# Optimization experiments

Measured on AMD Instinct MI355X. Metric: run time of the kernel, lower is better.

## Reference

```python
import jax, jax.numpy as jnp
import numpy as np

B, N_IN, D_IN, N_OUT, D_OUT, ROUTINGS = 512, 1152, 8, 10, 16, 3


def squash(s, axis=-1):
    # scale = |s|^2 / (1 + |s|^2) / (|s| + 1e-8)
    norm = jnp.linalg.norm(s, axis=axis, keepdims=True)
    return (norm ** 2 / (1.0 + norm ** 2) / (norm + 1e-8)) * s


def setup_inputs() -> dict:
    key = jax.random.key(0)
    k1, k2 = jax.random.split(key)
    x = jax.random.normal(k1, (B, N_IN, D_IN), dtype=jnp.float32)
    weight = 0.01 * jax.random.normal(k2, (N_OUT, N_IN, D_OUT, D_IN), dtype=jnp.float32)
    return {"x": x, "weight": weight}


def reference(x, weight):
    # x: [B, N_IN, D_IN]; weight: [N_OUT, N_IN, D_OUT, D_IN]
    # x_hat[b,o,n,:] = weight[o,n] @ x[b,n]  -> [B, N_OUT, N_IN, D_OUT]
    x_hat = jnp.einsum('onij,bnj->boni', weight, x)
    x_hat_det = jax.lax.stop_gradient(x_hat)

    # routing logits b: [B, N_OUT, N_IN]
    b = jnp.zeros(x_hat.shape[:3], dtype=x_hat.dtype)
    outputs = None
    for i in range(ROUTINGS):
        c = jax.nn.softmax(b, axis=1)  # softmax over output capsules
        if i == ROUTINGS - 1:
            outputs = squash(jnp.sum(c[..., None] * x_hat, axis=2))  # [B, N_OUT, D_OUT]
        else:
            outputs = squash(jnp.sum(c[..., None] * x_hat_det, axis=2))
            # agreement: b += <outputs, x_hat_det> over D_OUT
            b = b + jnp.einsum('bod,bond->bon', outputs, x_hat_det)
    return outputs  # [B, N_OUT, D_OUT]
```

## Files before the change

### kernel.cpp

```cpp
#include <hip/hip_runtime.h>
#include <hip/hip_bf16.h>
#include <hip/hip_fp16.h>

#define B_    512
#define NI    1152
#define NO    10
#define BT    16
#define NBT   32
#define NC    24
#define NCH   48
#define RNDS  6
#define RN    8

typedef __attribute__((ext_vector_type(8))) short bf16x8;
typedef __attribute__((ext_vector_type(4))) float f32x4;
typedef __attribute__((ext_vector_type(8))) unsigned short u16x8;

#define SPART_H    ((size_t)NC * NBT * NO * 256)
#define OUTSUM_F32 ((size_t)NBT * NO * 256)
#define XB_US      ((size_t)NBT * NC * RNDS * 1024)
#define WB_US      ((size_t)NC * RNDS * 12288)
#define WB2_US     ((size_t)NC * 12 * NO * 512)

__device__ inline unsigned short f2bf(float f) {
    __hip_bfloat16 h = __float2bfloat16(f);
    return *reinterpret_cast<unsigned short*>(&h);
}

__device__ __forceinline__ bf16x8 load_cvt8(const float* src) {
    f32x4 v0 = *reinterpret_cast<const f32x4*>(src);
    f32x4 v1 = *reinterpret_cast<const f32x4*>(src + 4);
    u16x8 u = { f2bf(v0[0]), f2bf(v0[1]), f2bf(v0[2]), f2bf(v0[3]),
                f2bf(v1[0]), f2bf(v1[1]), f2bf(v1[2]), f2bf(v1[3]) };
    return *reinterpret_cast<bf16x8*>(&u);
}

__device__ __forceinline__ void iter_epilogue(
    uint2 (*red)[NO * 64], const f32x4* sacc, float sc,
    int w, int l, int tid, unsigned short* base)
{
    #pragma unroll
    for (int o = 0; o < NO; ++o) {
        __half2 h01 = __floats2half2_rn(sacc[o][0] * sc, sacc[o][1] * sc);
        __half2 h23 = __floats2half2_rn(sacc[o][2] * sc, sacc[o][3] * sc);
        red[w][o * 64 + l] =
            make_uint2(*reinterpret_cast<unsigned int*>(&h01),
                       *reinterpret_cast<unsigned int*>(&h23));
    }
    __syncthreads();
    for (int g = tid; g < NO * 64; g += 256) {
        uint2 a0 = red[0][g], a1 = red[1][g], a2 = red[2][g], a3 = red[3][g];
        auto h2f2 = [](unsigned int u) {
            __half2 h = *reinterpret_cast<__half2*>(&u);
            return __half22float2(h);
        };
        float2 lo = h2f2(a0.x), l1 = h2f2(a1.x), l2 = h2f2(a2.x), l3 = h2f2(a3.x);
        float2 ho = h2f2(a0.y), h1 = h2f2(a1.y), h2 = h2f2(a2.y), h3 = h2f2(a3.y);
        float2 sl = { (lo.x + l1.x) + (l2.x + l3.x), (lo.y + l1.y) + (l2.y + l3.y) };
        float2 sh = { (ho.x + h1.x) + (h2.x + h3.x), (ho.y + h1.y) + (h2.y + h3.y) };
        __half2 p01 = __floats2half2_rn(sl.x, sl.y);
        __half2 p23 = __floats2half2_rn(sh.x, sh.y);
        *reinterpret_cast<uint2*>(base + (size_t)g * 4) =
            make_uint2(*reinterpret_cast<unsigned int*>(&p01),
                       *reinterpret_cast<unsigned int*>(&p23));
    }
}

__global__ __launch_bounds__(256) void cvt_xw(
    const float* __restrict__ x, const float* __restrict__ w,
    unsigned short* __restrict__ xb, unsigned short* __restrict__ wb,
    unsigned short* __restrict__ wb2)
{
    const int blk = blockIdx.x;
    if (blk < 2304) {
        const int t = blk * 256 + threadIdx.x;
        const int m   = t & 127;
        const int img = t >> 7;
        const int nl  = m >> 4, bl = m & 15;
        const int r   = img % RNDS;
        const int bc  = img / RNDS;
        const int nc  = bc % NC, bt = bc / NC;
        const int b   = bt * BT + bl;
        const int n   = nc * NCH + r * RN + nl;
        bf16x8 u = load_cvt8(x + ((size_t)b * NI + n) * 8);
        *reinterpret_cast<bf16x8*>(xb + (size_t)t * 8) = u;
    } else {
        const int t    = (blk - 2304) * 256 + threadIdx.x;
        const int lane = t & 63;
        const int gs   = (t >> 6) % 24;
        const int img  = t / 1536;
        const int h2   = lane >> 4, d = lane & 15;
        const int nl   = gs / 3, oq = gs % 3;
        const int r    = img % RNDS, nc = img / RNDS;
        const int o    = oq * 4 + h2;
        const int n    = nc * NCH + r * RN + nl;
        bf16x8 u = (bf16x8){0,0,0,0,0,0,0,0};
        if (o < NO) {
            u = load_cvt8(w + ((size_t)o * NI + n) * 128 + d * 8);
            const int g2  = r * 2 + (nl >> 2);
            const int hi2 = nl & 3;
            *reinterpret_cast<bf16x8*>(
                wb2 + (((size_t)nc * 12 + g2) * NO + o) * 512
                    + (hi2 * 16 + d) * 8) = u;
        }
        *reinterpret_cast<bf16x8*>(wb + (size_t)t * 8) = u;
    }
}

__global__ __launch_bounds__(256) void caps_it0(
    const unsigned short* __restrict__ xb,
    const unsigned short* __restrict__ wb2,
    unsigned short* __restrict__ s_part)
{
    __shared__ uint2 red[4][NO * 64];

    const int tid = threadIdx.x;
    const int wv  = tid >> 6;
    const int l   = tid & 63;
    const int b16 = l & 15;
    const int hi  = l >> 4;
    const int blk = blockIdx.x;
    const int xcd = blk & 7, idx = blk >> 3;
    const int nc  = xcd * 3 + (idx >> 5);
    const int bt  = idx & 31;

    f32x4 sacc[NO];
    #pragma unroll
    for (int o = 0; o < NO; ++o) sacc[o] = (f32x4){0.f, 0.f, 0.f, 0.f};

    const unsigned short* xbase = xb + (size_t)(bt * NC + nc) * (RNDS * 1024);
    const unsigned short* w2base = wb2 + (size_t)nc * (12 * NO * 512);

    #pragma unroll 1
    for (int gi = 0; gi < 3; ++gi) {
        const int g  = wv * 3 + gi;
        const int nn = 4 * g + hi;
        const int r  = nn >> 3, nl = nn & 7;
        bf16x8 bv4 = *reinterpret_cast<const bf16x8*>(
            xbase + (size_t)r * 1024 + (nl * 16 + b16) * 8);
        #pragma unroll
        for (int o = 0; o < NO; ++o) {
            bf16x8 av4 = *reinterpret_cast<const bf16x8*>(
                w2base + ((size_t)g * NO + o) * 512 + l * 8);
            sacc[o] = __builtin_amdgcn_mfma_f32_16x16x32_bf16(
                av4, bv4, sacc[o], 0, 0, 0);
        }
    }

    iter_epilogue(red, sacc, 0.1f, wv, l, tid,
                  s_part + ((size_t)nc * NBT + bt) * 2560);
}

__global__ __launch_bounds__(256, 3) void caps_itr(
    const unsigned short* __restrict__ xb,
    const unsigned short* __restrict__ wb,
    const float* __restrict__ outsum,
    unsigned short* __restrict__ s_part)
{
    __shared__ uint2 red[4][NO * 64];

    const int tid = threadIdx.x;
    const int wv  = tid >> 6;
    const int l   = tid & 63;
    const int b16 = l & 15;
    const int hi  = l >> 4;
    const int blk = blockIdx.x;
    const int xcd = blk & 7, idx = blk >> 3;
    const int nc  = xcd * 3 + (idx >> 5);
    const int bt  = idx & 31;

    f32x4 outf[NO];
    #pragma unroll
    for (int o = 0; o < NO; ++o)
        outf[o] = *reinterpret_cast<const f32x4*>(
            outsum + (((size_t)bt * NO + o) * 64 + l) * 4);

    f32x4 sacc[NO];
    #pragma unroll
    for (int o = 0; o < NO; ++o) sacc[o] = (f32x4){0.f, 0.f, 0.f, 0.f};

    const unsigned short* xbase = xb + (size_t)(bt * NC + nc) * (RNDS * 1024);
    const unsigned short* wbase = wb + (size_t)nc * (RNDS * 12288);

    auto bvp = [&](int g) {
        const int r = g >> 1, nl = wv * 2 + (g & 1);
        return reinterpret_cast<const bf16x8*>(
            xbase + (size_t)r * 1024 + nl * 128 + b16 * 8);
    };
    auto avp = [&](int g, int oq) {
        const int r = g >> 1, nl = wv * 2 + (g & 1);
        return reinterpret_cast<const bf16x8*>(
            wbase + (size_t)r * 12288 + (nl * 3 + oq) * 512 + l * 8);
    };

    const bf16x8 zero = {0,0,0,0,0,0,0,0};
    bf16x8 pb  = *bvp(0);
    bf16x8 pa0 = *avp(0, 0), pa1 = *avp(0, 1), pa2 = *avp(0, 2);

    #pragma unroll 1
    for (int g = 0; g < 2 * RNDS; ++g) {
        bf16x8 cb = pb;
        bf16x8 avv[3] = { pa0, pa1, pa2 };
        if (g + 1 < 2 * RNDS) {
            pb  = *bvp(g + 1);
            pa0 = *avp(g + 1, 0);
            pa1 = *avp(g + 1, 1);
            pa2 = *avp(g + 1, 2);
        }

        float lg[NO];
        #pragma unroll
        for (int oq = 0; oq < 3; ++oq) {
            const int tmax = (oq < 2) ? 4 : 2;
            #pragma unroll
            for (int t = 0; t < tmax; ++t) {
                const int o = oq * 4 + t;
                bf16x8 bvt = (hi == t) ? cb : zero;
                f32x4 xh = __builtin_amdgcn_mfma_f32_16x16x32_bf16(
                    avv[oq], bvt, (f32x4){0.f, 0.f, 0.f, 0.f}, 0, 0, 0);
                float pp = outf[o][0] * xh[0];
                pp = fmaf(outf[o][1], xh[1], pp);
                pp = fmaf(outf[o][2], xh[2], pp);
                pp = fmaf(outf[o][3], xh[3], pp);
                pp += __shfl_xor(pp, 16, 64);
                pp += __shfl_xor(pp, 32, 64);
                lg[o] = pp;
            }
        }
        float sum = 0.f;
        #pragma unroll
        for (int o = 0; o < NO; ++o) { lg[o] = __expf(lg[o]); sum += lg[o]; }
        const float rs = __builtin_amdgcn_rcpf(sum);
        #pragma unroll
        for (int o = 0; o < NO; ++o) lg[o] *= rs;

        #pragma unroll
        for (int oq = 0; oq < 3; ++oq) {
            const int tmax = (oq < 2) ? 4 : 2;
            #pragma unroll
            for (int t = 0; t < tmax; ++t) {
                const int o = oq * 4 + t;
                bf16x8 bvt = (hi == t) ? cb : zero;
                f32x4 xh = __builtin_amdgcn_mfma_f32_16x16x32_bf16(
                    avv[oq], bvt, (f32x4){0.f, 0.f, 0.f, 0.f}, 0, 0, 0);
                sacc[o][0] = fmaf(lg[o], xh[0], sacc[o][0]);
                sacc[o][1] = fmaf(lg[o], xh[1], sacc[o][1]);
                sacc[o][2] = fmaf(lg[o], xh[2], sacc[o][2]);
                sacc[o][3] = fmaf(lg[o], xh[3], sacc[o][3]);
            }
        }
    }

    iter_epilogue(red, sacc, 1.0f, wv, l, tid,
                  s_part + ((size_t)nc * NBT + bt) * 2560);
}

template<int MODE>
__global__ __launch_bounds__(256) void caps_squash(
    const unsigned short* __restrict__ s_part,
    float* __restrict__ outsum,
    float* __restrict__ dout)
{
    __shared__ float sq[256];
    const int bo = blockIdx.x;
    const int t  = threadIdx.x;

    float s = 0.f;
    #pragma unroll 4
    for (int nc = 0; nc < NC; ++nc) {
        __half h = *reinterpret_cast<const __half*>(
            s_part + ((size_t)nc * NBT * NO + bo) * 256 + t);
        s += __half2float(h);
    }

    float n2 = s * s;
    n2 += __shfl_xor(n2, 1, 64);
    n2 += __shfl_xor(n2, 2, 64);
    sq[t] = n2;
    __syncthreads();
    const int base = t & 63;
    n2 = (sq[base] + sq[64 + base]) + (sq[128 + base] + sq[192 + base]);

    const float norm  = sqrtf(n2);
    const float scale = n2 / ((1.f + n2) * (norm + 1e-8f));
    const float v = scale * s;

    if constexpr (MODE == 0) {
        outsum[(size_t)bo * 256 + t] = v;
    } else if constexpr (MODE == 1) {
        outsum[(size_t)bo * 256 + t] += v;
    } else {
        const int bt = bo / NO, o = bo - bt * NO;
        const int b16 = (t >> 2) & 15, hi = t >> 6, q = t & 3;
        dout[((size_t)(bt * BT + b16) * NO + o) * 16 + hi * 4 + q] = v;
    }
}

extern "C" void kernel_launch(void* const* d_in, const int* in_sizes, int n_in,
                              void* d_out, int out_size, void* d_ws, size_t ws_size,
                              hipStream_t stream) {
    const float* x = (const float*)d_in[0];
    const float* w = (const float*)d_in[1];
    float* out = (float*)d_out;

    unsigned short* s_part = (unsigned short*)d_ws;
    float*          outsum = (float*)(s_part + SPART_H);
    unsigned short* xb     = (unsigned short*)(outsum + OUTSUM_F32);
    unsigned short* wb     = xb + XB_US;
    unsigned short* wb2    = wb + WB_US;

    dim3 gI(NBT * NC), bI(256);
    dim3 gS(NBT * NO), bS(256);

    cvt_xw<<<dim3(3168), dim3(256), 0, stream>>>(x, w, xb, wb, wb2);
    caps_it0<<<gI, bI, 0, stream>>>(xb, wb2, s_part);
    caps_squash<0><<<gS, bS, 0, stream>>>(s_part, outsum, nullptr);
    caps_itr<<<gI, bI, 0, stream>>>(xb, wb, outsum, s_part);
    caps_squash<1><<<gS, bS, 0, stream>>>(s_part, outsum, nullptr);
    caps_itr<<<gI, bI, 0, stream>>>(xb, wb, outsum, s_part);
    caps_squash<2><<<gS, bS, 0, stream>>>(s_part, nullptr, out);
}
```

Measured before the change: 66.30 us.

## Split input capsules into 32 chunks of 36 and drop manual prefetch

Input capsules are now split into 32 chunks of 36 instead of 24 chunks of 48. That gives 1024 blocks (4 chunks per XCD), each doing less work, and the bf16 repack layout of x and weights is reshaped to match. The routing kernel drops its software-pipelined register prefetch for direct loads per step and raises its occupancy hint from 3 to 4. The aim is better CU occupancy and balance, at the cost of more partial sums to reduce and less latency hiding inside each wave.

```diff
diff --git a/kernel.cpp b/kernel.cpp
--- a/kernel.cpp
+++ b/kernel.cpp
@@ -7,10 +7,10 @@
 #define NO    10
 #define BT    16
 #define NBT   32
-#define NC    24
-#define NCH   48
-#define RNDS  6
-#define RN    8
+#define NC    32
+#define NCH   36
+#define NPW   9
+#define NG2   9
 
 typedef __attribute__((ext_vector_type(8))) short bf16x8;
 typedef __attribute__((ext_vector_type(4))) float f32x4;
@@ -18,9 +18,9 @@
 
 #define SPART_H    ((size_t)NC * NBT * NO * 256)
 #define OUTSUM_F32 ((size_t)NBT * NO * 256)
-#define XB_US      ((size_t)NBT * NC * RNDS * 1024)
-#define WB_US      ((size_t)NC * RNDS * 12288)
-#define WB2_US     ((size_t)NC * 12 * NO * 512)
+#define XB_US      ((size_t)NBT * NC * NCH * 128)
+#define WB_US      ((size_t)NC * NCH * 3 * 512)
+#define WB2_US     ((size_t)NC * NG2 * NO * 512)
 
 __device__ inline unsigned short f2bf(float f) {
     __hip_bfloat16 h = __float2bfloat16(f);
@@ -73,34 +73,32 @@
 {
     const int blk = blockIdx.x;
     if (blk < 2304) {
-        const int t = blk * 256 + threadIdx.x;
-        const int m   = t & 127;
-        const int img = t >> 7;
-        const int nl  = m >> 4, bl = m & 15;
-        const int r   = img % RNDS;
-        const int bc  = img / RNDS;
-        const int nc  = bc % NC, bt = bc / NC;
+        const int t   = blk * 256 + threadIdx.x;
+        const int img = t / 576;
+        const int m2  = t - img * 576;
+        const int nl  = m2 >> 4, bl = m2 & 15;
+        const int nc  = img % NC, bt = img / NC;
         const int b   = bt * BT + bl;
-        const int n   = nc * NCH + r * RN + nl;
+        const int n   = nc * NCH + nl;
         bf16x8 u = load_cvt8(x + ((size_t)b * NI + n) * 8);
         *reinterpret_cast<bf16x8*>(xb + (size_t)t * 8) = u;
     } else {
         const int t    = (blk - 2304) * 256 + threadIdx.x;
         const int lane = t & 63;
-        const int gs   = (t >> 6) % 24;
-        const int img  = t / 1536;
+        const int rest = t >> 6;
+        const int oq   = rest % 3;
+        const int rest2 = rest / 3;
+        const int nl   = rest2 % NCH, nc = rest2 / NCH;
         const int h2   = lane >> 4, d = lane & 15;
-        const int nl   = gs / 3, oq = gs % 3;
-        const int r    = img % RNDS, nc = img / RNDS;
         const int o    = oq * 4 + h2;
-        const int n    = nc * NCH + r * RN + nl;
+        const int n    = nc * NCH + nl;
         bf16x8 u = (bf16x8){0,0,0,0,0,0,0,0};
         if (o < NO) {
             u = load_cvt8(w + ((size_t)o * NI + n) * 128 + d * 8);
-            const int g2  = r * 2 + (nl >> 2);
+            const int g2  = nl >> 2;
             const int hi2 = nl & 3;
             *reinterpret_cast<bf16x8*>(
-                wb2 + (((size_t)nc * 12 + g2) * NO + o) * 512
+                wb2 + (((size_t)nc * NG2 + g2) * NO + o) * 512
                     + (hi2 * 16 + d) * 8) = u;
         }
         *reinterpret_cast<bf16x8*>(wb + (size_t)t * 8) = u;
@@ -121,23 +119,23 @@
     const int hi  = l >> 4;
     const int blk = blockIdx.x;
     const int xcd = blk & 7, idx = blk >> 3;
-    const int nc  = xcd * 3 + (idx >> 5);
+    const int nc  = xcd * 4 + (idx >> 5);
     const int bt  = idx & 31;
 
     f32x4 sacc[NO];
     #pragma unroll
     for (int o = 0; o < NO; ++o) sacc[o] = (f32x4){0.f, 0.f, 0.f, 0.f};
 
-    const unsigned short* xbase = xb + (size_t)(bt * NC + nc) * (RNDS * 1024);
-    const unsigned short* w2base = wb2 + (size_t)nc * (12 * NO * 512);
+    const unsigned short* xbase  = xb  + (size_t)(bt * NC + nc) * (NCH * 128);
+    const unsigned short* w2base = wb2 + (size_t)nc * (NG2 * NO * 512);
 
     #pragma unroll 1
     for (int gi = 0; gi < 3; ++gi) {
-        const int g  = wv * 3 + gi;
-        const int nn = 4 * g + hi;
-        const int r  = nn >> 3, nl = nn & 7;
+        const int g = wv + gi * 4;
+        if (g >= NG2) break;
+        const int nl = g * 4 + hi;
         bf16x8 bv4 = *reinterpret_cast<const bf16x8*>(
-            xbase + (size_t)r * 1024 + (nl * 16 + b16) * 8);
+            xbase + nl * 128 + b16 * 8);
         #pragma unroll
         for (int o = 0; o < NO; ++o) {
             bf16x8 av4 = *reinterpret_cast<const bf16x8*>(
@@ -151,7 +149,7 @@
                   s_part + ((size_t)nc * NBT + bt) * 2560);
 }
 
-__global__ __launch_bounds__(256, 3) void caps_itr(
+__global__ __launch_bounds__(256, 4) void caps_itr(
     const unsigned short* __restrict__ xb,
     const unsigned short* __restrict__ wb,
     const float* __restrict__ outsum,
@@ -166,7 +164,7 @@
     const int hi  = l >> 4;
     const int blk = blockIdx.x;
     const int xcd = blk & 7, idx = blk >> 3;
-    const int nc  = xcd * 3 + (idx >> 5);
+    const int nc  = xcd * 4 + (idx >> 5);
     const int bt  = idx & 31;
 
     f32x4 outf[NO];
@@ -179,34 +177,21 @@
     #pragma unroll
     for (int o = 0; o < NO; ++o) sacc[o] = (f32x4){0.f, 0.f, 0.f, 0.f};
 
-    const unsigned short* xbase = xb + (size_t)(bt * NC + nc) * (RNDS * 1024);
-    const unsigned short* wbase = wb + (size_t)nc * (RNDS * 12288);
-
-    auto bvp = [&](int g) {
-        const int r = g >> 1, nl = wv * 2 + (g & 1);
-        return reinterpret_cast<const bf16x8*>(
-            xbase + (size_t)r * 1024 + nl * 128 + b16 * 8);
-    };
-    auto avp = [&](int g, int oq) {
-        const int r = g >> 1, nl = wv * 2 + (g & 1);
-        return reinterpret_cast<const bf16x8*>(
-            wbase + (size_t)r * 12288 + (nl * 3 + oq) * 512 + l * 8);
-    };
+    const unsigned short* xbase = xb + (size_t)(bt * NC + nc) * (NCH * 128);
+    const unsigned short* wbase = wb + (size_t)nc * (NCH * 3 * 512);
 
     const bf16x8 zero = {0,0,0,0,0,0,0,0};
-    bf16x8 pb  = *bvp(0);
-    bf16x8 pa0 = *avp(0, 0), pa1 = *avp(0, 1), pa2 = *avp(0, 2);
 
     #pragma unroll 1
-    for (int g = 0; g < 2 * RNDS; ++g) {
-        bf16x8 cb = pb;
-        bf16x8 avv[3] = { pa0, pa1, pa2 };
-        if (g + 1 < 2 * RNDS) {
-            pb  = *bvp(g + 1);
-            pa0 = *avp(g + 1, 0);
-            pa1 = *avp(g + 1, 1);
-            pa2 = *avp(g + 1, 2);
-        }
+    for (int g = 0; g < NPW; ++g) {
+        const int nl = wv * NPW + g;
+        bf16x8 bv = *reinterpret_cast<const bf16x8*>(
+            xbase + nl * 128 + b16 * 8);
+        bf16x8 avv[3];
+        #pragma unroll
+        for (int oq = 0; oq < 3; ++oq)
+            avv[oq] = *reinterpret_cast<const bf16x8*>(
+                wbase + (nl * 3 + oq) * 512 + l * 8);
 
         float lg[NO];
         #pragma unroll
@@ -215,7 +200,7 @@
             #pragma unroll
             for (int t = 0; t < tmax; ++t) {
                 const int o = oq * 4 + t;
-                bf16x8 bvt = (hi == t) ? cb : zero;
+                bf16x8 bvt = (hi == t) ? bv : zero;
                 f32x4 xh = __builtin_amdgcn_mfma_f32_16x16x32_bf16(
                     avv[oq], bvt, (f32x4){0.f, 0.f, 0.f, 0.f}, 0, 0, 0);
                 float pp = outf[o][0] * xh[0];
@@ -240,7 +225,7 @@
             #pragma unroll
             for (int t = 0; t < tmax; ++t) {
                 const int o = oq * 4 + t;
-                bf16x8 bvt = (hi == t) ? cb : zero;
+                bf16x8 bvt = (hi == t) ? bv : zero;
                 f32x4 xh = __builtin_amdgcn_mfma_f32_16x16x32_bf16(
                     avv[oq], bvt, (f32x4){0.f, 0.f, 0.f, 0.f}, 0, 0, 0);
                 sacc[o][0] = fmaf(lg[o], xh[0], sacc[o][0]);
```

Measured after the change: 90.99 us. 1.37x slower.
